# Kernel tuning notes

Measured on AMD Instinct MI355X. Metric: run time of the kernel, lower is better.

The kernel has to match this reference:

```python
import jax, jax.numpy as jnp
import numpy as np

IN = 128          # in_channels
STEPS = 3         # processing_steps


def setup_inputs() -> dict:
    key = jax.random.key(0)
    ks = jax.random.split(key, 6)
    N, B = 500000, 1024
    x = jax.random.normal(ks[0], (N, IN), dtype=jnp.float32)
    batch = jnp.sort(jax.random.randint(ks[1], (N,), 0, B)).astype(jnp.int64)
    s = 1.0 / np.sqrt(IN)  # PyTorch LSTM init range
    w_ih = jax.random.uniform(ks[2], (4 * IN, 2 * IN), jnp.float32, -s, s)
    w_hh = jax.random.uniform(ks[3], (4 * IN, IN), jnp.float32, -s, s)
    b_ih = jax.random.uniform(ks[4], (4 * IN,), jnp.float32, -s, s)
    b_hh = jax.random.uniform(ks[5], (4 * IN,), jnp.float32, -s, s)
    return {"x": x, "w_ih": w_ih, "w_hh": w_hh, "b_ih": b_ih, "b_hh": b_hh,
            "batch": batch, "batch_size": B}


def reference(x, w_ih, w_hh, b_ih, b_hh, batch, batch_size):
    h = jnp.zeros((batch_size, IN), x.dtype)
    c = jnp.zeros((batch_size, IN), x.dtype)
    q_star = jnp.zeros((batch_size, 2 * IN), x.dtype)
    for _ in range(STEPS):
        # single-layer LSTM step (PyTorch gate order: i, f, g, o)
        gates = q_star @ w_ih.T + b_ih + h @ w_hh.T + b_hh
        i, f, g, o = jnp.split(gates, 4, axis=-1)
        c = jax.nn.sigmoid(f) * c + jax.nn.sigmoid(i) * jnp.tanh(g)
        h = jax.nn.sigmoid(o) * jnp.tanh(c)
        q = h  # [B, IN]
        # per-graph segment softmax over attention scores
        e = jnp.sum(x * q[batch], axis=-1)                       # [N]
        m = jax.ops.segment_max(e, batch, num_segments=batch_size)
        ex = jnp.exp(e - m[batch])
        denom = jax.ops.segment_sum(ex, batch, num_segments=batch_size)
        a = ex / denom[batch]                                    # [N]
        # weighted segment-sum readout
        r = jax.ops.segment_sum(x * a[:, None], batch, num_segments=batch_size)
        q_star = jnp.concatenate([q, r], axis=-1)                # [B, 2*IN]
    return q_star
```

## Files before the change

kernel.cpp:

```cpp
#include <hip/hip_runtime.h>
#include <math.h>

#define IN_CH 128
#define G4    512
#define K1    256
#define SPLIT 4

__device__ __forceinline__ float sigmoidf_(float v){ return 1.f/(1.f + expf(-v)); }

__device__ __forceinline__ float dot4_(float4 a, float4 b){
  return a.x*b.x + a.y*b.y + a.z*b.z + a.w*b.w;
}

__device__ __forceinline__ float reduce16_(float v){
  int t;
  t = __builtin_amdgcn_update_dpp(0, __float_as_int(v), 0xB1, 0xF, 0xF, true);
  v += __int_as_float(t);
  t = __builtin_amdgcn_update_dpp(0, __float_as_int(v), 0x4E, 0xF, 0xF, true);
  v += __int_as_float(t);
  t = __builtin_amdgcn_update_dpp(0, __float_as_int(v), 0x141, 0xF, 0xF, true);
  v += __int_as_float(t);
  t = __builtin_amdgcn_update_dpp(0, __float_as_int(v), 0x140, 0xF, 0xF, true);
  v += __int_as_float(t);
  return v;
}

__device__ __forceinline__ float swz16_(float v){
  return __int_as_float(__builtin_amdgcn_ds_swizzle(__float_as_int(v), 0x401F));
}

__global__ void prologue_kernel(const float* __restrict__ w_ih, const float* __restrict__ w_hh,
                                float* __restrict__ wTih, float* __restrict__ wThh,
                                const int* __restrict__ batch, int N, int B, int* __restrict__ segs,
                                const float* __restrict__ b_ih, const float* __restrict__ b_hh,
                                float* __restrict__ h, float* __restrict__ c, float* __restrict__ qstar){
  int blk = blockIdx.x;
  if (blk < 512){
    int idx = blk*256 + threadIdx.x;
    { int g = idx / K1; int k = idx - g*K1; wTih[k*G4 + g] = w_ih[idx]; }
    if (idx < G4*IN_CH){ int g = idx / IN_CH; int k = idx - g*IN_CH; wThh[k*G4 + g] = w_hh[idx]; }
  } else if (blk < 517){
    int b = (blk - 512)*256 + threadIdx.x;
    if (b > B) return;
    if (b == B){ segs[B] = N; return; }
    int lo = 0, hi = N;
    while (lo < hi){ int mid = (lo + hi) >> 1; if (batch[mid] < b) lo = mid + 1; else hi = mid; }
    segs[b] = lo;
  } else {
    int idx = (blk - 517)*256 + threadIdx.x;
    if (idx >= B*IN_CH) return;
    int b = idx >> 7, ch = idx & 127;
    float iv = sigmoidf_(b_ih[ch]           + b_hh[ch]);
    float gv = tanhf    (b_ih[2*IN_CH + ch] + b_hh[2*IN_CH + ch]);
    float ov = sigmoidf_(b_ih[3*IN_CH + ch] + b_hh[3*IN_CH + ch]);
    float cv = iv*gv;
    float hv = ov*tanhf(cv);
    c[idx] = cv; h[idx] = hv;
    qstar[b*K1 + ch] = hv;
  }
}

__global__ __launch_bounds__(512) void lstm_fused_kernel(
    const float* __restrict__ qstar, const float* __restrict__ pm, const float* __restrict__ pd,
    const float* __restrict__ pr, float* __restrict__ h, float* __restrict__ c,
    const float* __restrict__ wTih, const float* __restrict__ wThh,
    const float* __restrict__ b_ih, const float* __restrict__ b_hh,
    float* __restrict__ qstar_out){
  int g    = threadIdx.x;
  int row0 = blockIdx.x*8;
  __shared__ float qs[8][K1];
  __shared__ float hs[8][IN_CH];
  __shared__ float gs[8][G4];
  for (int t = g; t < 8*IN_CH; t += 512){ int r = t >> 7; int k = t & 127; qs[r][k] = qstar[(row0+r)*K1 + k]; }
  for (int t = g; t < 8*IN_CH; t += 512){
    int r = t >> 7, ch = t & 127; int b = row0 + r;
    float m0 = pm[b*SPLIT+0], m1 = pm[b*SPLIT+1], m2 = pm[b*SPLIT+2], m3 = pm[b*SPLIT+3];
    float M = fmaxf(fmaxf(m0, m1), fmaxf(m2, m3));
    float f0 = (M == -INFINITY) ? 0.f : __expf(m0 - M);
    float f1 = (M == -INFINITY) ? 0.f : __expf(m1 - M);
    float f2 = (M == -INFINITY) ? 0.f : __expf(m2 - M);
    float f3 = (M == -INFINITY) ? 0.f : __expf(m3 - M);
    float dd = pd[b*SPLIT+0]*f0 + pd[b*SPLIT+1]*f1 + pd[b*SPLIT+2]*f2 + pd[b*SPLIT+3]*f3;
    float rr = pr[(size_t)(b*SPLIT+0)*IN_CH + ch]*f0 + pr[(size_t)(b*SPLIT+1)*IN_CH + ch]*f1
             + pr[(size_t)(b*SPLIT+2)*IN_CH + ch]*f2 + pr[(size_t)(b*SPLIT+3)*IN_CH + ch]*f3;
    qs[r][IN_CH + ch] = (dd > 0.f) ? rr/dd : 0.f;
  }
  for (int t = g; t < 8*IN_CH; t += 512){ int r = t >> 7; int k = t & 127; hs[r][k] = h[(row0+r)*IN_CH + k]; }
  __syncthreads();
  float bias = b_ih[g] + b_hh[g];
  float acc[8];
#pragma unroll
  for (int r = 0; r < 8; ++r) acc[r] = bias;
  for (int k4 = 0; k4 < K1/4; ++k4){
    float w0 = wTih[(4*k4+0)*G4 + g];
    float w1 = wTih[(4*k4+1)*G4 + g];
    float w2 = wTih[(4*k4+2)*G4 + g];
    float w3 = wTih[(4*k4+3)*G4 + g];
#pragma unroll
    for (int r = 0; r < 8; ++r){
      float4 q = *reinterpret_cast<const float4*>(&qs[r][4*k4]);
      acc[r] += q.x*w0 + q.y*w1 + q.z*w2 + q.w*w3;
    }
  }
  for (int k4 = 0; k4 < IN_CH/4; ++k4){
    float w0 = wThh[(4*k4+0)*G4 + g];
    float w1 = wThh[(4*k4+1)*G4 + g];
    float w2 = wThh[(4*k4+2)*G4 + g];
    float w3 = wThh[(4*k4+3)*G4 + g];
#pragma unroll
    for (int r = 0; r < 8; ++r){
      float4 hv = *reinterpret_cast<const float4*>(&hs[r][4*k4]);
      acc[r] += hv.x*w0 + hv.y*w1 + hv.z*w2 + hv.w*w3;
    }
  }
#pragma unroll
  for (int r = 0; r < 8; ++r) gs[r][g] = acc[r];
  __syncthreads();
  for (int t = g; t < 8*IN_CH; t += 512){
    int r = t >> 7, ch = t & 127;
    int idx = (row0+r)*IN_CH + ch;
    float iv = sigmoidf_(gs[r][ch]);
    float fv = sigmoidf_(gs[r][IN_CH + ch]);
    float gv = tanhf(gs[r][2*IN_CH + ch]);
    float ov = sigmoidf_(gs[r][3*IN_CH + ch]);
    float cv = fv*c[idx] + iv*gv;
    float hv = ov*tanhf(cv);
    c[idx] = cv; h[idx] = hv;
    qstar_out[(row0+r)*K1 + ch] = hv;
  }
}

__global__ __launch_bounds__(256) void attn_part_kernel(const float* __restrict__ x,
    const float* __restrict__ qstar, const int* __restrict__ segs,
    float* __restrict__ pm, float* __restrict__ pd, float* __restrict__ pr){
  int b = blockIdx.x, p = blockIdx.y;
  int s = segs[b], t = segs[b+1];
  int len = t - s;
  int cs = s + (int)(((long long)len * p) / SPLIT);
  int ce = s + (int)(((long long)len * (p+1)) / SPLIT);
  int tid = threadIdx.x;
  int wave = tid >> 6, lane = tid & 63;
  int grp = (lane >> 4) & 3, l16 = lane & 15;
  int sid = wave*4 + grp;
  const float4 z4 = make_float4(0.f,0.f,0.f,0.f);
  const float4* x4 = reinterpret_cast<const float4*>(x);
  const float4* q4 = reinterpret_cast<const float4*>(&qstar[(size_t)b*K1]);
  float4 qa = q4[l16], qb = q4[16 + l16];

  float m = -INFINITY, d = 0.f;
  float4 ra = z4, rb = z4;

  for (int j0 = cs + sid*2; j0 < ce; j0 += 32){
    int j1 = j0 + 1;
    bool ok1 = (j1 < ce);
    const float4* r0 = x4 + (size_t)j0*(IN_CH/4);
    const float4* r1 = x4 + (size_t)j1*(IN_CH/4);
    float4 a0 = r0[l16],        b0 = r0[16 + l16];
    float4 a1 = ok1 ? r1[l16] : z4, b1 = ok1 ? r1[16 + l16] : z4;
    float e0 = dot4_(a0, qa) + dot4_(b0, qb);
    float e1 = dot4_(a1, qa) + dot4_(b1, qb);
    e0 = reduce16_(e0);
    e1 = reduce16_(e1);
    e1 = ok1 ? e1 : -INFINITY;
    float em = fmaxf(e0, e1);
    if (em > m){
      float corr = __expf(m - em);
      d *= corr;
      ra.x *= corr; ra.y *= corr; ra.z *= corr; ra.w *= corr;
      rb.x *= corr; rb.y *= corr; rb.z *= corr; rb.w *= corr;
      m = em;
    }
    float p0 = __expf(e0 - m);
    float p1 = __expf(e1 - m);
    d += p0 + p1;
    ra.x += p0*a0.x + p1*a1.x; ra.y += p0*a0.y + p1*a1.y;
    ra.z += p0*a0.z + p1*a1.z; ra.w += p0*a0.w + p1*a1.w;
    rb.x += p0*b0.x + p1*b1.x; rb.y += p0*b0.y + p1*b1.y;
    rb.z += p0*b0.z + p1*b1.z; rb.w += p0*b0.w + p1*b1.w;
  }
  {
    float mo = swz16_(m), dd = swz16_(d);
    float4 rao, rbo;
    rao.x = swz16_(ra.x); rao.y = swz16_(ra.y); rao.z = swz16_(ra.z); rao.w = swz16_(ra.w);
    rbo.x = swz16_(rb.x); rbo.y = swz16_(rb.y); rbo.z = swz16_(rb.z); rbo.w = swz16_(rb.w);
    float mn = fmaxf(m, mo);
    float c1 = (mn == -INFINITY) ? 0.f : __expf(m - mn);
    float c2 = (mn == -INFINITY) ? 0.f : __expf(mo - mn);
    d = d*c1 + dd*c2;
    ra.x = ra.x*c1 + rao.x*c2; ra.y = ra.y*c1 + rao.y*c2;
    ra.z = ra.z*c1 + rao.z*c2; ra.w = ra.w*c1 + rao.w*c2;
    rb.x = rb.x*c1 + rbo.x*c2; rb.y = rb.y*c1 + rbo.y*c2;
    rb.z = rb.z*c1 + rbo.z*c2; rb.w = rb.w*c1 + rbo.w*c2;
    m = mn;
  }
  {
    float mo = __shfl_xor(m, 32), dd = __shfl_xor(d, 32);
    float4 rao, rbo;
    rao.x = __shfl_xor(ra.x, 32); rao.y = __shfl_xor(ra.y, 32);
    rao.z = __shfl_xor(ra.z, 32); rao.w = __shfl_xor(ra.w, 32);
    rbo.x = __shfl_xor(rb.x, 32); rbo.y = __shfl_xor(rb.y, 32);
    rbo.z = __shfl_xor(rb.z, 32); rbo.w = __shfl_xor(rb.w, 32);
    float mn = fmaxf(m, mo);
    float c1 = (mn == -INFINITY) ? 0.f : __expf(m - mn);
    float c2 = (mn == -INFINITY) ? 0.f : __expf(mo - mn);
    d = d*c1 + dd*c2;
    ra.x = ra.x*c1 + rao.x*c2; ra.y = ra.y*c1 + rao.y*c2;
    ra.z = ra.z*c1 + rao.z*c2; ra.w = ra.w*c1 + rao.w*c2;
    rb.x = rb.x*c1 + rbo.x*c2; rb.y = rb.y*c1 + rbo.y*c2;
    rb.z = rb.z*c1 + rbo.z*c2; rb.w = rb.w*c1 + rbo.w*c2;
    m = mn;
  }
  __shared__ float mbuf[4], dbuf[4];
  __shared__ float rbA[4][64], rbB[4][64];
  if (lane < 16){
    *reinterpret_cast<float4*>(&rbA[wave][l16*4]) = ra;
    *reinterpret_cast<float4*>(&rbB[wave][l16*4]) = rb;
    if (l16 == 0){ mbuf[wave] = m; dbuf[wave] = d; }
  }
  __syncthreads();
  int part = b*SPLIT + p;
  if (tid < IN_CH){
    float M = fmaxf(fmaxf(mbuf[0], mbuf[1]), fmaxf(mbuf[2], mbuf[3]));
    float f0 = (M == -INFINITY) ? 0.f : __expf(mbuf[0] - M);
    float f1 = (M == -INFINITY) ? 0.f : __expf(mbuf[1] - M);
    float f2 = (M == -INFINITY) ? 0.f : __expf(mbuf[2] - M);
    float f3 = (M == -INFINITY) ? 0.f : __expf(mbuf[3] - M);
    float v0 = (tid < 64) ? rbA[0][tid] : rbB[0][tid-64];
    float v1 = (tid < 64) ? rbA[1][tid] : rbB[1][tid-64];
    float v2 = (tid < 64) ? rbA[2][tid] : rbB[2][tid-64];
    float v3 = (tid < 64) ? rbA[3][tid] : rbB[3][tid-64];
    pr[(size_t)part*IN_CH + tid] = v0*f0 + v1*f1 + v2*f2 + v3*f3;
    if (tid == 0){
      pd[part] = dbuf[0]*f0 + dbuf[1]*f1 + dbuf[2]*f2 + dbuf[3]*f3;
      pm[part] = M;
    }
  }
}

__global__ void attn_combine_kernel(const float* __restrict__ pm, const float* __restrict__ pd,
                                    const float* __restrict__ pr, float* __restrict__ qstar){
  int b = blockIdx.x; int ch = threadIdx.x;
  float M = -INFINITY;
#pragma unroll
  for (int p = 0; p < SPLIT; ++p) M = fmaxf(M, pm[b*SPLIT + p]);
  float d = 0.f, r = 0.f;
#pragma unroll
  for (int p = 0; p < SPLIT; ++p){
    float mp = pm[b*SPLIT + p];
    float f = (mp == -INFINITY) ? 0.f : __expf(mp - M);
    d += pd[b*SPLIT + p] * f;
    r += pr[(size_t)(b*SPLIT + p)*IN_CH + ch] * f;
  }
  qstar[b*K1 + IN_CH + ch] = (d > 0.f) ? r/d : 0.f;
}

extern "C" void kernel_launch(void* const* d_in, const int* in_sizes, int n_in,
                              void* d_out, int out_size, void* d_ws, size_t ws_size,
                              hipStream_t stream){
  const float* x     = (const float*)d_in[0];
  const float* w_ih  = (const float*)d_in[1];
  const float* w_hh  = (const float*)d_in[2];
  const float* b_ih  = (const float*)d_in[3];
  const float* b_hh  = (const float*)d_in[4];
  const int*   batch = (const int*)d_in[5];
  int N = in_sizes[0] / IN_CH;
  int B = out_size / K1;
  float* out = (float*)d_out;

  float* ws    = (float*)d_ws;
  float* h     = ws;
  float* c     = h + (size_t)B*IN_CH;
  float* wTih  = c + (size_t)B*IN_CH;
  float* wThh  = wTih + K1*G4;
  int*   segs  = (int*)(wThh + IN_CH*G4);
  float* pm    = (float*)(segs + (B + 2));
  float* pd    = pm + (size_t)B*SPLIT;
  float* pr    = pd + (size_t)B*SPLIT;

  prologue_kernel<<<517 + (B*IN_CH + 255)/256, 256, 0, stream>>>(
      w_ih, w_hh, wTih, wThh, batch, N, B, segs, b_ih, b_hh, h, c, out);

  attn_part_kernel<<<dim3(B, SPLIT), 256, 0, stream>>>(x, out, segs, pm, pd, pr);
  for (int step = 1; step < 3; ++step){
    lstm_fused_kernel<<<B/8, 512, 0, stream>>>(out, pm, pd, pr, h, c, wTih, wThh, b_ih, b_hh, out);
    attn_part_kernel<<<dim3(B, SPLIT), 256, 0, stream>>>(x, out, segs, pm, pd, pr);
  }
  attn_combine_kernel<<<B, IN_CH, 0, stream>>>(pm, pd, pr, out);
}
```

Baseline: 202.3 us.

## Drop split-segment attention partials; one block per graph with register prefetch

Removes the SPLIT=4 partitioning of each graph's node range, the partial max/denominator/readout buffers, and the final combine kernel. Each graph is now handled by a single 256-thread block that writes the normalized readout straight into q_star, and the LSTM kernel reads q_star directly. The node loop gains software prefetch of the next pair of rows into registers so loads overlap the current dot products. The trade-off is four times fewer attention blocks (1024 instead of 4096), so each block walks a longer serial chain and the GPU has less parallelism to hide memory latency.

```diff
diff --git a/kernel.cpp b/kernel.cpp
--- a/kernel.cpp
+++ b/kernel.cpp
@@ -4,7 +4,6 @@
 #define IN_CH 128
 #define G4    512
 #define K1    256
-#define SPLIT 4
 
 __device__ __forceinline__ float sigmoidf_(float v){ return 1.f/(1.f + expf(-v)); }
 
@@ -61,8 +60,7 @@
 }
 
 __global__ __launch_bounds__(512) void lstm_fused_kernel(
-    const float* __restrict__ qstar, const float* __restrict__ pm, const float* __restrict__ pd,
-    const float* __restrict__ pr, float* __restrict__ h, float* __restrict__ c,
+    const float* __restrict__ qstar_in, float* __restrict__ h, float* __restrict__ c,
     const float* __restrict__ wTih, const float* __restrict__ wThh,
     const float* __restrict__ b_ih, const float* __restrict__ b_hh,
     float* __restrict__ qstar_out){
@@ -71,20 +69,7 @@
   __shared__ float qs[8][K1];
   __shared__ float hs[8][IN_CH];
   __shared__ float gs[8][G4];
-  for (int t = g; t < 8*IN_CH; t += 512){ int r = t >> 7; int k = t & 127; qs[r][k] = qstar[(row0+r)*K1 + k]; }
-  for (int t = g; t < 8*IN_CH; t += 512){
-    int r = t >> 7, ch = t & 127; int b = row0 + r;
-    float m0 = pm[b*SPLIT+0], m1 = pm[b*SPLIT+1], m2 = pm[b*SPLIT+2], m3 = pm[b*SPLIT+3];
-    float M = fmaxf(fmaxf(m0, m1), fmaxf(m2, m3));
-    float f0 = (M == -INFINITY) ? 0.f : __expf(m0 - M);
-    float f1 = (M == -INFINITY) ? 0.f : __expf(m1 - M);
-    float f2 = (M == -INFINITY) ? 0.f : __expf(m2 - M);
-    float f3 = (M == -INFINITY) ? 0.f : __expf(m3 - M);
-    float dd = pd[b*SPLIT+0]*f0 + pd[b*SPLIT+1]*f1 + pd[b*SPLIT+2]*f2 + pd[b*SPLIT+3]*f3;
-    float rr = pr[(size_t)(b*SPLIT+0)*IN_CH + ch]*f0 + pr[(size_t)(b*SPLIT+1)*IN_CH + ch]*f1
-             + pr[(size_t)(b*SPLIT+2)*IN_CH + ch]*f2 + pr[(size_t)(b*SPLIT+3)*IN_CH + ch]*f3;
-    qs[r][IN_CH + ch] = (dd > 0.f) ? rr/dd : 0.f;
-  }
+  for (int t = g; t < 8*K1; t += 512){ int r = t >> 8; int k = t & 255; qs[r][k] = qstar_in[(row0+r)*K1 + k]; }
   for (int t = g; t < 8*IN_CH; t += 512){ int r = t >> 7; int k = t & 127; hs[r][k] = h[(row0+r)*IN_CH + k]; }
   __syncthreads();
   float bias = b_ih[g] + b_hh[g];
@@ -130,14 +115,10 @@
   }
 }
 
-__global__ __launch_bounds__(256) void attn_part_kernel(const float* __restrict__ x,
-    const float* __restrict__ qstar, const int* __restrict__ segs,
-    float* __restrict__ pm, float* __restrict__ pd, float* __restrict__ pr){
-  int b = blockIdx.x, p = blockIdx.y;
-  int s = segs[b], t = segs[b+1];
-  int len = t - s;
-  int cs = s + (int)(((long long)len * p) / SPLIT);
-  int ce = s + (int)(((long long)len * (p+1)) / SPLIT);
+__global__ __launch_bounds__(256) void attn_kernel(const float* __restrict__ x,
+    float* __restrict__ qstar, const int* __restrict__ segs){
+  int b = blockIdx.x;
+  int s = segs[b], ce = segs[b+1];
   int tid = threadIdx.x;
   int wave = tid >> 6, lane = tid & 63;
   int grp = (lane >> 4) & 3, l16 = lane & 15;
@@ -150,13 +131,22 @@
   float m = -INFINITY, d = 0.f;
   float4 ra = z4, rb = z4;
 
-  for (int j0 = cs + sid*2; j0 < ce; j0 += 32){
-    int j1 = j0 + 1;
-    bool ok1 = (j1 < ce);
-    const float4* r0 = x4 + (size_t)j0*(IN_CH/4);
-    const float4* r1 = x4 + (size_t)j1*(IN_CH/4);
-    float4 a0 = r0[l16],        b0 = r0[16 + l16];
-    float4 a1 = ok1 ? r1[l16] : z4, b1 = ok1 ? r1[16 + l16] : z4;
+  int j = s + sid*2;
+  float4 a0 = z4, b0 = z4, a1 = z4, b1 = z4;
+  if (j < ce){
+    const float4* r0 = x4 + (size_t)j*(IN_CH/4);
+    a0 = r0[l16]; b0 = r0[16 + l16];
+    if (j + 1 < ce){ a1 = r0[32 + l16]; b1 = r0[48 + l16]; }
+  }
+  while (j < ce){
+    int jn = j + 32;
+    float4 na0 = z4, nb0 = z4, na1 = z4, nb1 = z4;
+    if (jn < ce){
+      const float4* rn = x4 + (size_t)jn*(IN_CH/4);
+      na0 = rn[l16]; nb0 = rn[16 + l16];
+      if (jn + 1 < ce){ na1 = rn[32 + l16]; nb1 = rn[48 + l16]; }
+    }
+    bool ok1 = (j + 1 < ce);
     float e0 = dot4_(a0, qa) + dot4_(b0, qb);
     float e1 = dot4_(a1, qa) + dot4_(b1, qb);
     e0 = reduce16_(e0);
@@ -177,6 +167,8 @@
     ra.z += p0*a0.z + p1*a1.z; ra.w += p0*a0.w + p1*a1.w;
     rb.x += p0*b0.x + p1*b1.x; rb.y += p0*b0.y + p1*b1.y;
     rb.z += p0*b0.z + p1*b1.z; rb.w += p0*b0.w + p1*b1.w;
+    j = jn;
+    a0 = na0; b0 = nb0; a1 = na1; b1 = nb1;
   }
   {
     float mo = swz16_(m), dd = swz16_(d);
@@ -218,7 +210,6 @@
     if (l16 == 0){ mbuf[wave] = m; dbuf[wave] = d; }
   }
   __syncthreads();
-  int part = b*SPLIT + p;
   if (tid < IN_CH){
     float M = fmaxf(fmaxf(mbuf[0], mbuf[1]), fmaxf(mbuf[2], mbuf[3]));
     float f0 = (M == -INFINITY) ? 0.f : __expf(mbuf[0] - M);
@@ -229,29 +220,10 @@
     float v1 = (tid < 64) ? rbA[1][tid] : rbB[1][tid-64];
     float v2 = (tid < 64) ? rbA[2][tid] : rbB[2][tid-64];
     float v3 = (tid < 64) ? rbA[3][tid] : rbB[3][tid-64];
-    pr[(size_t)part*IN_CH + tid] = v0*f0 + v1*f1 + v2*f2 + v3*f3;
-    if (tid == 0){
-      pd[part] = dbuf[0]*f0 + dbuf[1]*f1 + dbuf[2]*f2 + dbuf[3]*f3;
-      pm[part] = M;
-    }
-  }
-}
-
-__global__ void attn_combine_kernel(const float* __restrict__ pm, const float* __restrict__ pd,
-                                    const float* __restrict__ pr, float* __restrict__ qstar){
-  int b = blockIdx.x; int ch = threadIdx.x;
-  float M = -INFINITY;
-#pragma unroll
-  for (int p = 0; p < SPLIT; ++p) M = fmaxf(M, pm[b*SPLIT + p]);
-  float d = 0.f, r = 0.f;
-#pragma unroll
-  for (int p = 0; p < SPLIT; ++p){
-    float mp = pm[b*SPLIT + p];
-    float f = (mp == -INFINITY) ? 0.f : __expf(mp - M);
-    d += pd[b*SPLIT + p] * f;
-    r += pr[(size_t)(b*SPLIT + p)*IN_CH + ch] * f;
-  }
-  qstar[b*K1 + IN_CH + ch] = (d > 0.f) ? r/d : 0.f;
+    float R = v0*f0 + v1*f1 + v2*f2 + v3*f3;
+    float D = dbuf[0]*f0 + dbuf[1]*f1 + dbuf[2]*f2 + dbuf[3]*f3;
+    qstar[(size_t)b*K1 + IN_CH + tid] = (D > 0.f) ? R/D : 0.f;
+  }
 }
 
 extern "C" void kernel_launch(void* const* d_in, const int* in_sizes, int n_in,
@@ -273,17 +245,13 @@
   float* wTih  = c + (size_t)B*IN_CH;
   float* wThh  = wTih + K1*G4;
   int*   segs  = (int*)(wThh + IN_CH*G4);
-  float* pm    = (float*)(segs + (B + 2));
-  float* pd    = pm + (size_t)B*SPLIT;
-  float* pr    = pd + (size_t)B*SPLIT;
 
   prologue_kernel<<<517 + (B*IN_CH + 255)/256, 256, 0, stream>>>(
       w_ih, w_hh, wTih, wThh, batch, N, B, segs, b_ih, b_hh, h, c, out);
 
-  attn_part_kernel<<<dim3(B, SPLIT), 256, 0, stream>>>(x, out, segs, pm, pd, pr);
+  attn_kernel<<<B, 256, 0, stream>>>(x, out, segs);
   for (int step = 1; step < 3; ++step){
-    lstm_fused_kernel<<<B/8, 512, 0, stream>>>(out, pm, pd, pr, h, c, wTih, wThh, b_ih, b_hh, out);
-    attn_part_kernel<<<dim3(B, SPLIT), 256, 0, stream>>>(x, out, segs, pm, pd, pr);
-  }
-  attn_combine_kernel<<<B, IN_CH, 0, stream>>>(pm, pd, pr, out);
-}
+    lstm_fused_kernel<<<B/8, 512, 0, stream>>>(out, h, c, wTih, wThh, b_ih, b_hh, out);
+    attn_kernel<<<B, 256, 0, stream>>>(x, out, segs);
+  }
+}
```

Measured after the change: 206.6 us. 2.2% more time.
